# Optimization experiments

Measured on AMD Instinct MI355X. Metric: run time of the kernel, lower is better.

Reference implementation:

```python
import jax, jax.numpy as jnp
import numpy as np

B, T, D, H, NB, K, CDIM, CTX = 8, 4096, 3, 128, 6, 20, 128, 7


def setup_inputs() -> dict:
    key = jax.random.key(0)
    ks = jax.random.split(key, 16)
    s = 0.05
    inp = {
        'p': jax.random.normal(ks[0], (B, T, D), jnp.float32),
        'W_pos': jax.random.normal(ks[1], (D, H), jnp.float32) * s,
        'b_pos': jnp.zeros((H,), jnp.float32),
        # ResnetBlockFC(2H -> H): fc_0(2H,H), fc_1(H,H), shortcut(2H,H, no bias)
        'blk_W0': jax.random.normal(ks[2], (NB, 2 * H, H), jnp.float32) * s,
        'blk_b0': jnp.zeros((NB, H), jnp.float32),
        'blk_W1': jax.random.normal(ks[3], (NB, H, H), jnp.float32) * s,
        'blk_b1': jnp.zeros((NB, H), jnp.float32),
        'blk_Ws': jax.random.normal(ks[4], (NB, 2 * H, H), jnp.float32) * s,
        # Attention: score MLP on context (dim 7 -> 1), output proj (H -> H)
        'att_Wc': jax.random.normal(ks[5], (NB, CTX, 1), jnp.float32) * s,
        'att_bc': jnp.zeros((NB, 1), jnp.float32),
        'att_Wo': jax.random.normal(ks[6], (NB, H, H), jnp.float32) * s,
        'att_bo': jnp.zeros((NB, H), jnp.float32),
        'W_c': jax.random.normal(ks[7], (H, CDIM), jnp.float32) * s,
        'b_c': jnp.zeros((CDIM,), jnp.float32),
    }
    return inp


def _knn(p):
    # squared pairwise distances [B,T,T], top-K smallest
    sq = jnp.sum(p * p, axis=-1)  # [B,T]
    d2 = sq[:, :, None] + sq[:, None, :] - 2.0 * jnp.einsum('btd,bsd->bts', p, p)
    neg, idx = jax.lax.top_k(-d2, K)            # idx: [B,T,K]
    dis = jnp.sqrt(jnp.maximum(-neg, 1e-12))    # euclidean distance [B,T,K]
    return dis, idx


def _gather(c, idx):
    # c: [B,T,h], idx: [B,T,K] -> [B,T,K,h]  (vectorized pool_local)
    return jax.vmap(lambda ci, ii: ci[ii])(c, idx)


def _resnet_block(x, W0, b0, W1, b1, Ws):
    # occupancy-networks ResnetBlockFC: shortcut(x) + fc_1(relu(fc_0(relu(x))))
    h = jnp.maximum(x, 0.0) @ W0 + b0
    dx = jnp.maximum(h, 0.0) @ W1 + b1
    return x @ Ws + dx


def reference(p, W_pos, b_pos, blk_W0, blk_b0, blk_W1, blk_b1, blk_Ws,
              att_Wc, att_bc, att_Wo, att_bo, W_c, b_c):
    dis, idx = _knn(p)
    pooled_points = _gather(p, idx)                                   # [B,T,K,3]
    p_rep = jnp.broadcast_to(p[:, :, None, :], (B, T, K, D))
    context = jnp.concatenate([dis[..., None], pooled_points, p_rep], axis=-1)  # [B,T,K,7]

    net = p @ W_pos + b_pos                                           # [B,T,H]
    last_net = jnp.zeros_like(net)
    for i in range(NB):
        pooled = _gather(net, idx)                                    # [B,T,K,H]
        # attention over the K neighbors, weights from context
        scores = context @ att_Wc[i] + att_bc[i]                      # [B,T,K,1]
        w = jax.nn.softmax(scores, axis=2)
        att = jnp.sum(w * pooled, axis=2) @ att_Wo[i] + att_bo[i]     # [B,T,H]
        x = jnp.concatenate([net, att], axis=2)                       # [B,T,2H]
        net = _resnet_block(x, blk_W0[i], blk_b0[i], blk_W1[i], blk_b1[i], blk_Ws[i])
        net = net + last_net
        last_net = net
    return net @ W_c + b_c                                            # [B,T,c_dim]
```

## Files before the change

kernel.cpp:

```cpp
#include <hip/hip_runtime.h>
#include <hip/hip_bf16.h>
#include <math.h>

#define BB 8
#define TT 4096
#define HHD 128
#define NBK 6
#define KNN 20
#define BT (BB*TT)

typedef __attribute__((ext_vector_type(8))) short bf16x8;
typedef __attribute__((ext_vector_type(4))) float f32x4;

__device__ __forceinline__ float b2f(unsigned short u){
  return __uint_as_float(((unsigned int)u) << 16);
}
__device__ __forceinline__ unsigned short f2b(float f){
  unsigned int x = __float_as_uint(f);
  unsigned int r = (x + 0x7fffu + ((x >> 16) & 1u)) >> 16;
  return (unsigned short)r;
}
__device__ __forceinline__ float ldp(const void* base, int i, int f32m){
  return f32m ? ((const float*)base)[i] : b2f(((const unsigned short*)base)[i]);
}
__device__ __forceinline__ float lo2f(unsigned int u){ return __uint_as_float(u << 16); }
__device__ __forceinline__ float hi2f(unsigned int u){ return __uint_as_float(u & 0xffff0000u); }
__device__ __forceinline__ unsigned int relu2(unsigned int u){
  unsigned int s = u & 0x80008000u;
  unsigned int m = s | (s - (s >> 15));
  return u & ~m;
}
__device__ __forceinline__ bf16x8 relu8(bf16x8 x){
  union { bf16x8 v; unsigned int u[4]; } t; t.v = x;
  t.u[0] = relu2(t.u[0]); t.u[1] = relu2(t.u[1]);
  t.u[2] = relu2(t.u[2]); t.u[3] = relu2(t.u[3]);
  return t.v;
}

__global__ void k_detect(const unsigned short* __restrict__ wpos_raw, int* __restrict__ flag){
  int lane = threadIdx.x;
  int cnt = 0;
  for (int i = lane; i < 384; i += 64) {
    unsigned int e = (wpos_raw[i] >> 7) & 0xFFu;
    if (e >= 0x90u) cnt++;
  }
  #pragma unroll
  for (int off = 32; off > 0; off >>= 1) cnt += __shfl_down(cnt, off);
  if (lane == 0) *flag = (cnt > 10) ? 1 : 0;
}

__global__ __launch_bounds__(256) void k_prep_points(const void* __restrict__ p,
                                                     const int* __restrict__ flagp,
                                                     float4* __restrict__ pf4){
  int r = blockIdx.x*256 + threadIdx.x;
  if (r >= BT) return;
  int f32m = *flagp;
  float x = ldp(p, r*3+0, f32m), y = ldp(p, r*3+1, f32m), z = ldp(p, r*3+2, f32m);
  float sq = __fadd_rn(__fadd_rn(__fmul_rn(x,x), __fmul_rn(y,y)), __fmul_rn(z,z));
  pf4[r] = make_float4(x, y, z, sq);
}

__global__ __launch_bounds__(256) void k_net0(const float4* __restrict__ pf4,
                                              const void* __restrict__ Wpos,
                                              const void* __restrict__ bpos,
                                              const int* __restrict__ flagp,
                                              unsigned short* __restrict__ netA){
  int t = blockIdx.x*256 + threadIdx.x;
  int f32m = *flagp;
  int c = t & 127, r = t >> 7;
  float4 q = pf4[r];
  float v = ldp(bpos, c, f32m);
  v = fmaf(q.x, ldp(Wpos, c,       f32m), v);
  v = fmaf(q.y, ldp(Wpos, 128 + c, f32m), v);
  v = fmaf(q.z, ldp(Wpos, 256 + c, f32m), v);
  netA[t] = f2b(v);
}

__global__ __launch_bounds__(256) void k_transpose(const void* __restrict__ W0,
                                                   const void* __restrict__ W1,
                                                   const void* __restrict__ Ws,
                                                   const void* __restrict__ Wo,
                                                   const void* __restrict__ Wc,
                                                   const int* __restrict__ flagp,
                                                   unsigned short* __restrict__ wT){
  int t = blockIdx.x*256 + threadIdx.x;
  int f32m = *flagp;
  if (t < 196608) {
    int i = t >> 15; int rem = t & 32767; int n = rem >> 8; int k = rem & 255;
    wT[t] = f2b(ldp(W0, i*32768 + k*128 + n, f32m));
  } else if (t < 294912) {
    int u = t - 196608; int i = u >> 14; int rem = u & 16383; int n = rem >> 7; int k = rem & 127;
    wT[t] = f2b(ldp(W1, i*16384 + k*128 + n, f32m));
  } else if (t < 491520) {
    int u = t - 294912; int i = u >> 15; int rem = u & 32767; int n = rem >> 8; int k = rem & 255;
    wT[t] = f2b(ldp(Ws, i*32768 + k*128 + n, f32m));
  } else if (t < 589824) {
    int u = t - 491520; int i = u >> 14; int rem = u & 16383; int n = rem >> 7; int k = rem & 127;
    wT[t] = f2b(ldp(Wo, i*16384 + k*128 + n, f32m));
  } else if (t < 606208) {
    int u = t - 589824; int n = u >> 7; int k = u & 127;
    wT[t] = f2b(ldp(Wc, k*128 + n, f32m));
  }
}

#define INS(act, dv, iv) do { bool A_ = (act); float D_ = (dv); int I_ = (iv);        \
  _Pragma("unroll")                                                                    \
  for (int j = 19; j >= 1; --j) {                                                      \
    bool cj = A_ && (D_ < ld[j]); bool cm = A_ && (D_ < ld[j-1]);                      \
    ld[j] = cj ? (cm ? ld[j-1] : D_) : ld[j];                                          \
    li[j] = cj ? (cm ? li[j-1] : I_) : li[j];                                          \
  }                                                                                    \
  { bool c0 = A_ && (D_ < ld[0]); ld[0] = c0 ? D_ : ld[0]; li[0] = c0 ? I_ : li[0]; } \
} while(0)

#define KCAP 22

__global__ __launch_bounds__(256) void k_knn(const float4* __restrict__ pf4,
                                             const void* __restrict__ Wc,
                                             const void* __restrict__ bc,
                                             const int* __restrict__ flagp,
                                             unsigned short* __restrict__ idx16,
                                             unsigned short* __restrict__ wsoftb){
  __shared__ __align__(16) char smem[16384 + KCAP*2048];
  __shared__ unsigned int sthr[64];
  float4* tile = (float4*)smem;
  float*  lsd  = (float*)smem;
  int*    lsi  = (int*)(smem + 20480);
  float2* stk  = (float2*)(smem + 16384);

  int tid  = threadIdx.x;
  int part = tid >> 6, lane = tid & 63;
  int rq   = blockIdx.x*64 + lane;
  int b    = rq >> 12;
  int f32m = *flagp;
  float4 q = pf4[rq];

  if (tid < 64) sthr[tid] = 0x7F7FFFFFu;

  float ld[20]; int li[20];
  #pragma unroll
  for (int j = 0; j < 20; ++j) { ld[j] = 3.0e38f; li[j] = 0; }
  float thresh = 3.0e38f;
  int cnt = 0;

  for (int ch = 0; ch < 4; ++ch) {
    __syncthreads();
    {
      const float4* src = pf4 + (b << 12) + part*1024 + ch*256;
      tile[part*256 + lane      ] = src[lane      ];
      tile[part*256 + lane +  64] = src[lane +  64];
      tile[part*256 + lane + 128] = src[lane + 128];
      tile[part*256 + lane + 192] = src[lane + 192];
    }
    __syncthreads();
    thresh = fminf(thresh, __uint_as_float(sthr[lane]));
    int baseI = part*1024 + ch*256;
    #pragma unroll 4
    for (int j = 0; j < 256; ++j) {
      float4 pt = tile[part*256 + j];
      float dot = __fadd_rn(__fadd_rn(__fmul_rn(q.x,pt.x), __fmul_rn(q.y,pt.y)),
                            __fmul_rn(q.z,pt.z));
      float d2  = __fsub_rn(__fadd_rn(q.w, pt.w), __fmul_rn(2.0f, dot));
      if (d2 < thresh) {
        stk[cnt*256 + tid] = make_float2(d2, __int_as_float(baseI + j));
        cnt++;
      }
      if (__ballot(cnt >= KCAP)) {
        #pragma unroll 1
        for (int u = 0; u < KCAP; ++u) {
          float2 e = stk[u*256 + tid];
          INS(u < cnt, e.x, __float_as_int(e.y));
        }
        cnt = 0;
        atomicMin(&sthr[lane], __float_as_uint(fmaxf(ld[19], 0.0f)));
        thresh = fminf(ld[19], __uint_as_float(sthr[lane]));
      }
    }
  }
  {
    int mc = cnt;
    #pragma unroll
    for (int o = 32; o > 0; o >>= 1) mc = max(mc, __shfl_xor(mc, o));
    #pragma unroll 1
    for (int u = 0; u < mc; ++u) {
      float2 e = stk[u*256 + tid];
      INS(u < cnt, e.x, __float_as_int(e.y));
    }
  }

  __syncthreads();
  #pragma unroll
  for (int j = 0; j < 20; ++j) { lsd[tid*20 + j] = ld[j]; lsi[tid*20 + j] = li[j]; }
  __syncthreads();

  if (tid < 64) {
    int p0 = tid*20, p1 = (64+tid)*20, p2 = (128+tid)*20, p3 = (192+tid)*20;
    int i0=0, i1=0, i2=0, i3=0;
    float dis[20]; int outi[20];
    #pragma unroll 4
    for (int o = 0; o < 20; ++o) {
      float d0 = lsd[p0+i0], d1 = lsd[p1+i1], d2v = lsd[p2+i2], d3 = lsd[p3+i3];
      float bd = d0; int sel = 0;
      if (d1  < bd) { bd = d1;  sel = 1; }
      if (d2v < bd) { bd = d2v; sel = 2; }
      if (d3  < bd) { bd = d3;  sel = 3; }
      int bi = (sel==0) ? lsi[p0+i0] : (sel==1) ? lsi[p1+i1] : (sel==2) ? lsi[p2+i2] : lsi[p3+i3];
      i0 += (sel==0); i1 += (sel==1); i2 += (sel==2); i3 += (sel==3);
      dis[o] = sqrtf(fmaxf(bd, 1e-12f));
      outi[o] = bi;
    }
    float nx[20], ny[20], nz[20];
    #pragma unroll 4
    for (int k = 0; k < 20; ++k) {
      idx16[rq*20 + k] = (unsigned short)outi[k];
      float4 pp = pf4[(b << 12) + outi[k]];
      nx[k] = pp.x; ny[k] = pp.y; nz[k] = pp.z;
    }
    for (int i = 0; i < NBK; ++i) {
      float w0 = ldp(Wc,i*7+0,f32m), w1 = ldp(Wc,i*7+1,f32m), w2 = ldp(Wc,i*7+2,f32m);
      float w3 = ldp(Wc,i*7+3,f32m), w4 = ldp(Wc,i*7+4,f32m), w5 = ldp(Wc,i*7+5,f32m);
      float w6 = ldp(Wc,i*7+6,f32m);
      float bci = ldp(bc,i,f32m);
      float s[20]; float mx = -3.0e38f;
      #pragma unroll
      for (int k = 0; k < 20; ++k) {
        float v = bci;
        v = fmaf(dis[k], w0, v);
        v = fmaf(nx[k], w1, v); v = fmaf(ny[k], w2, v); v = fmaf(nz[k], w3, v);
        v = fmaf(q.x, w4, v);  v = fmaf(q.y, w5, v);  v = fmaf(q.z, w6, v);
        s[k] = v; mx = fmaxf(mx, v);
      }
      float sum = 0.f;
      #pragma unroll
      for (int k = 0; k < 20; ++k) { float e = __expf(s[k] - mx); s[k] = e; sum += e; }
      float inv = 1.0f / sum;
      #pragma unroll
      for (int k = 0; k < 20; ++k) wsoftb[(rq*6 + i)*20 + k] = f2b(s[k]*inv);
    }
  }
}

__global__ __launch_bounds__(256) void k_block(const unsigned short* __restrict__ netIn,
                                               unsigned short* __restrict__ netOut,
                                               const unsigned short* __restrict__ idx16,
                                               const unsigned short* __restrict__ wsoftb,
                                               const unsigned short* __restrict__ wT,
                                               const void* __restrict__ b0s,
                                               const void* __restrict__ b1s,
                                               const void* __restrict__ bos,
                                               const int* __restrict__ flagp,
                                               int iblk, int hasResid){
  __shared__ unsigned short ldsA[2][16*136];
  __shared__ unsigned short ldsH[2][16*136];
  int tid = threadIdx.x;
  int f32m = *flagp;
  int w = tid >> 6, lane = tid & 63;
  int t = w >> 1;
  int c = w & 1;
  int b  = blockIdx.x & 7;
  int r0 = (b << 12) + ((blockIdx.x >> 3) << 5) + (t << 4);
  const unsigned short* W0T = wT + iblk*32768;
  const unsigned short* W1T = wT + 196608 + iblk*16384;
  const unsigned short* WsT = wT + 294912 + iblk*32768;
  const unsigned short* WoT = wT + 491520 + iblk*16384;
  int m = lane & 15, qd = lane >> 4;

  {
    int r = lane >> 2, cg = lane & 3;
    int grow = r0 + r;
    int cbase = c*64 + cg*16;
    const unsigned int* ip = (const unsigned int*)(idx16 + grow*20);
    const unsigned int* wp = (const unsigned int*)(wsoftb + (grow*6 + iblk)*20);
    unsigned int iv[10], wv[10];
    #pragma unroll
    for (int j = 0; j < 10; ++j) iv[j] = ip[j];
    #pragma unroll
    for (int j = 0; j < 10; ++j) wv[j] = wp[j];
    float acc[16];
    #pragma unroll
    for (int j = 0; j < 16; ++j) acc[j] = 0.f;
    #pragma unroll 4
    for (int k = 0; k < 20; ++k) {
      unsigned int pair = iv[k >> 1];
      int nb = (int)((k & 1) ? (pair >> 16) : pair) & 4095;
      unsigned int wpair = wv[k >> 1];
      float wk = (k & 1) ? hi2f(wpair) : lo2f(wpair);
      const uint4* np_ = (const uint4*)(netIn + ((b << 12) + nb)*128 + cbase);
      #pragma unroll
      for (int u = 0; u < 2; ++u) {
        uint4 uu = np_[u];
        acc[u*8+0] = fmaf(wk, lo2f(uu.x), acc[u*8+0]);
        acc[u*8+1] = fmaf(wk, hi2f(uu.x), acc[u*8+1]);
        acc[u*8+2] = fmaf(wk, lo2f(uu.y), acc[u*8+2]);
        acc[u*8+3] = fmaf(wk, hi2f(uu.y), acc[u*8+3]);
        acc[u*8+4] = fmaf(wk, lo2f(uu.z), acc[u*8+4]);
        acc[u*8+5] = fmaf(wk, hi2f(uu.z), acc[u*8+5]);
        acc[u*8+6] = fmaf(wk, lo2f(uu.w), acc[u*8+6]);
        acc[u*8+7] = fmaf(wk, hi2f(uu.w), acc[u*8+7]);
      }
    }
    unsigned short* hb = ldsH[t];
    #pragma unroll
    for (int j = 0; j < 8; ++j) {
      unsigned int pr = ((unsigned int)f2b(acc[2*j+1]) << 16) | (unsigned int)f2b(acc[2*j]);
      *(unsigned int*)(hb + r*136 + cbase + 2*j) = pr;
    }
  }
  __syncthreads();

  {
    bf16x8 asf[4];
    #pragma unroll
    for (int ks = 0; ks < 4; ++ks)
      asf[ks] = *(const bf16x8*)(ldsH[t] + m*136 + ks*32 + qd*8);
    f32x4 acc2[4];
    #pragma unroll
    for (int i = 0; i < 4; ++i) { f32x4 z = {0.f,0.f,0.f,0.f}; acc2[i] = z; }
    #pragma unroll
    for (int i = 0; i < 4; ++i) {
      int cti = c*4 + i;
      const unsigned short* bp = WoT + (cti*16 + m)*128 + qd*8;
      #pragma unroll
      for (int ks = 0; ks < 4; ++ks)
        acc2[i] = __builtin_amdgcn_mfma_f32_16x16x32_bf16(asf[ks], *(const bf16x8*)(bp + ks*32), acc2[i], 0, 0, 0);
    }
    unsigned short* ab = ldsA[t];
    #pragma unroll
    for (int i = 0; i < 4; ++i) {
      int col = (c*4 + i)*16 + m;
      float bo = ldp(bos, iblk*128 + col, f32m);
      #pragma unroll
      for (int rr = 0; rr < 4; ++rr)
        ab[(qd*4 + rr)*136 + col] = f2b(acc2[i][rr] + bo);
    }
  }
  __syncthreads();

  bf16x8 nf[4], af[4];
  {
    const unsigned short* nrow = netIn + (r0 + m)*128;
    #pragma unroll
    for (int ks = 0; ks < 4; ++ks) nf[ks] = *(const bf16x8*)(nrow + ks*32 + qd*8);
    #pragma unroll
    for (int ks = 0; ks < 4; ++ks) af[ks] = *(const bf16x8*)(ldsA[t] + m*136 + ks*32 + qd*8);
    bf16x8 rnf[4], raf[4];
    #pragma unroll
    for (int ks = 0; ks < 4; ++ks) { rnf[ks] = relu8(nf[ks]); raf[ks] = relu8(af[ks]); }
    f32x4 acc3[4];
    #pragma unroll
    for (int i = 0; i < 4; ++i) { f32x4 z = {0.f,0.f,0.f,0.f}; acc3[i] = z; }
    #pragma unroll
    for (int i = 0; i < 4; ++i) {
      int cti = c*4 + i;
      const unsigned short* bp = W0T + (cti*16 + m)*256 + qd*8;
      #pragma unroll
      for (int ks = 0; ks < 4; ++ks)
        acc3[i] = __builtin_amdgcn_mfma_f32_16x16x32_bf16(rnf[ks], *(const bf16x8*)(bp + ks*32), acc3[i], 0, 0, 0);
      #pragma unroll
      for (int ks = 0; ks < 4; ++ks)
        acc3[i] = __builtin_amdgcn_mfma_f32_16x16x32_bf16(raf[ks], *(const bf16x8*)(bp + 128 + ks*32), acc3[i], 0, 0, 0);
    }
    unsigned short* hb = ldsH[t];
    #pragma unroll
    for (int i = 0; i < 4; ++i) {
      int col = (c*4 + i)*16 + m;
      float b0v = ldp(b0s, iblk*128 + col, f32m);
      #pragma unroll
      for (int rr = 0; rr < 4; ++rr)
        hb[(qd*4 + rr)*136 + col] = f2b(fmaxf(acc3[i][rr] + b0v, 0.f));
    }
  }
  __syncthreads();

  {
    bf16x8 hf[4];
    #pragma unroll
    for (int ks = 0; ks < 4; ++ks) hf[ks] = *(const bf16x8*)(ldsH[t] + m*136 + ks*32 + qd*8);
    f32x4 acc4[4];
    #pragma unroll
    for (int i = 0; i < 4; ++i) { f32x4 z = {0.f,0.f,0.f,0.f}; acc4[i] = z; }
    #pragma unroll
    for (int i = 0; i < 4; ++i) {
      int cti = c*4 + i;
      const unsigned short* bp1 = W1T + (cti*16 + m)*128 + qd*8;
      #pragma unroll
      for (int ks = 0; ks < 4; ++ks)
        acc4[i] = __builtin_amdgcn_mfma_f32_16x16x32_bf16(hf[ks], *(const bf16x8*)(bp1 + ks*32), acc4[i], 0, 0, 0);
      const unsigned short* bps = WsT + (cti*16 + m)*256 + qd*8;
      #pragma unroll
      for (int ks = 0; ks < 4; ++ks)
        acc4[i] = __builtin_amdgcn_mfma_f32_16x16x32_bf16(nf[ks], *(const bf16x8*)(bps + ks*32), acc4[i], 0, 0, 0);
      #pragma unroll
      for (int ks = 0; ks < 4; ++ks)
        acc4[i] = __builtin_amdgcn_mfma_f32_16x16x32_bf16(af[ks], *(const bf16x8*)(bps + 128 + ks*32), acc4[i], 0, 0, 0);
    }
    #pragma unroll
    for (int i = 0; i < 4; ++i) {
      int col = (c*4 + i)*16 + m;
      float b1v = ldp(b1s, iblk*128 + col, f32m);
      #pragma unroll
      for (int rr = 0; rr < 4; ++rr) {
        int grow2 = r0 + qd*4 + rr;
        float v = acc4[i][rr] + b1v;
        if (hasResid) v += b2f(netIn[grow2*128 + col]);
        netOut[grow2*128 + col] = f2b(v);
      }
    }
  }
}

__global__ __launch_bounds__(256) void k_final(const unsigned short* __restrict__ netIn,
                                               const unsigned short* __restrict__ WcT,
                                               const void* __restrict__ bcv,
                                               const int* __restrict__ flagp,
                                               void* __restrict__ out){
  int tid = threadIdx.x; int w = tid >> 6, lane = tid & 63;
  int f32m = *flagp;
  int t = w >> 1, c = w & 1;
  int r0 = blockIdx.x*32 + t*16;
  int m = lane & 15, qd = lane >> 4;
  bf16x8 nf[4];
  #pragma unroll
  for (int ks = 0; ks < 4; ++ks)
    nf[ks] = *(const bf16x8*)(netIn + (r0 + m)*128 + ks*32 + qd*8);
  f32x4 acc[4];
  #pragma unroll
  for (int i = 0; i < 4; ++i) { f32x4 z = {0.f,0.f,0.f,0.f}; acc[i] = z; }
  #pragma unroll
  for (int i = 0; i < 4; ++i) {
    int cti = c*4 + i;
    const unsigned short* bp = WcT + (cti*16 + m)*128 + qd*8;
    #pragma unroll
    for (int ks = 0; ks < 4; ++ks)
      acc[i] = __builtin_amdgcn_mfma_f32_16x16x32_bf16(nf[ks], *(const bf16x8*)(bp + ks*32), acc[i], 0, 0, 0);
  }
  if (f32m) {
    float* o = (float*)out;
    #pragma unroll
    for (int i = 0; i < 4; ++i) {
      int col = (c*4 + i)*16 + m;
      float bcf = ldp(bcv, col, 1);
      #pragma unroll
      for (int rr = 0; rr < 4; ++rr)
        o[(r0 + qd*4 + rr)*128 + col] = acc[i][rr] + bcf;
    }
  } else {
    unsigned short* o = (unsigned short*)out;
    #pragma unroll
    for (int i = 0; i < 4; ++i) {
      int col = (c*4 + i)*16 + m;
      float bcf = ldp(bcv, col, 0);
      #pragma unroll
      for (int rr = 0; rr < 4; ++rr)
        o[(r0 + qd*4 + rr)*128 + col] = f2b(acc[i][rr] + bcf);
    }
  }
}

extern "C" void kernel_launch(void* const* d_in, const int* in_sizes, int n_in,
                              void* d_out, int out_size, void* d_ws, size_t ws_size,
                              hipStream_t stream){
  const void* p    = d_in[0];
  const void* Wpos = d_in[1];
  const void* bpos = d_in[2];
  const void* W0   = d_in[3];
  const void* b0   = d_in[4];
  const void* W1   = d_in[5];
  const void* b1   = d_in[6];
  const void* Ws   = d_in[7];
  const void* Wc_  = d_in[8];
  const void* bc_  = d_in[9];
  const void* Wo   = d_in[10];
  const void* bo   = d_in[11];
  const void* WC   = d_in[12];
  const void* bC   = d_in[13];

  char* ws = (char*)d_ws;
  int*            flag   = (int*)(ws + 0);
  float4*         pf4    = (float4*)(ws + 256);
  unsigned short* idx16  = (unsigned short*)(ws + 524544);
  unsigned short* wsoftb = (unsigned short*)(ws + 1835264);
  unsigned short* netA   = (unsigned short*)(ws + 9699584);
  unsigned short* wT     = (unsigned short*)(ws + 18088192);

  k_detect     <<<dim3(1),     dim3(64),  0, stream>>>((const unsigned short*)Wpos, flag);
  k_prep_points<<<dim3(128),   dim3(256), 0, stream>>>(p, flag, pf4);
  k_net0       <<<dim3(16384), dim3(256), 0, stream>>>(pf4, Wpos, bpos, flag, netA);
  k_transpose  <<<dim3(2368),  dim3(256), 0, stream>>>(W0, W1, Ws, Wo, WC, flag, wT);
  k_knn        <<<dim3(512),   dim3(256), 0, stream>>>(pf4, Wc_, bc_, flag, idx16, wsoftb);

  unsigned short* a   = netA;
  unsigned short* bpt = (unsigned short*)d_out;
  for (int i = 0; i < 6; ++i) {
    k_block<<<dim3(1024), dim3(256), 0, stream>>>(a, bpt, idx16, wsoftb, wT,
                                                  b0, b1, bo, flag, i, (i > 0) ? 1 : 0);
    unsigned short* t = a; a = bpt; bpt = t;
  }
  k_final<<<dim3(1024), dim3(256), 0, stream>>>(a, wT + 589824, bC, flag, d_out);
}
```

Before: 646.0 us.

## Split KNN candidate scan across eight wave partitions with compact LDS stacks

The KNN kernel now runs 512 threads per block, so each query's 4096 candidates are scanned by eight waves of 512 points instead of four waves of 1024, halving the serial scan per thread. The candidate stack is split into separate float distance and 16-bit index arrays with a smaller capacity. The flush check now runs once per four candidates, so the stack fills half as often. The final merge becomes 8-way, and shared memory is repacked to fit in about 62 KB. The trade-offs are a longer merge, more LDS per block, and more frequent stack flushes from the smaller capacity.

```diff
diff --git a/kernel.cpp b/kernel.cpp
--- a/kernel.cpp
+++ b/kernel.cpp
@@ -113,20 +113,21 @@
   { bool c0 = A_ && (D_ < ld[0]); ld[0] = c0 ? D_ : ld[0]; li[0] = c0 ? I_ : li[0]; } \
 } while(0)
 
-#define KCAP 22
-
-__global__ __launch_bounds__(256) void k_knn(const float4* __restrict__ pf4,
+#define KCAP 10
+
+__global__ __launch_bounds__(512) void k_knn(const float4* __restrict__ pf4,
                                              const void* __restrict__ Wc,
                                              const void* __restrict__ bc,
                                              const int* __restrict__ flagp,
                                              unsigned short* __restrict__ idx16,
                                              unsigned short* __restrict__ wsoftb){
-  __shared__ __align__(16) char smem[16384 + KCAP*2048];
+  __shared__ __align__(16) char smem[63488];
   __shared__ unsigned int sthr[64];
-  float4* tile = (float4*)smem;
-  float*  lsd  = (float*)smem;
-  int*    lsi  = (int*)(smem + 20480);
-  float2* stk  = (float2*)(smem + 16384);
+  float4*         tile  = (float4*)smem;
+  float*          stkd  = (float*)(smem + 32768);
+  unsigned short* stki  = (unsigned short*)(smem + 53248);
+  float*          lsd   = (float*)smem;
+  unsigned short* lsi16 = (unsigned short*)(smem + 40960);
 
   int tid  = threadIdx.x;
   int part = tid >> 6, lane = tid & 63;
@@ -143,10 +144,10 @@
   float thresh = 3.0e38f;
   int cnt = 0;
 
-  for (int ch = 0; ch < 4; ++ch) {
+  for (int ch = 0; ch < 2; ++ch) {
     __syncthreads();
     {
-      const float4* src = pf4 + (b << 12) + part*1024 + ch*256;
+      const float4* src = pf4 + (b << 12) + part*512 + ch*256;
       tile[part*256 + lane      ] = src[lane      ];
       tile[part*256 + lane +  64] = src[lane +  64];
       tile[part*256 + lane + 128] = src[lane + 128];
@@ -154,22 +155,27 @@
     }
     __syncthreads();
     thresh = fminf(thresh, __uint_as_float(sthr[lane]));
-    int baseI = part*1024 + ch*256;
-    #pragma unroll 4
-    for (int j = 0; j < 256; ++j) {
-      float4 pt = tile[part*256 + j];
-      float dot = __fadd_rn(__fadd_rn(__fmul_rn(q.x,pt.x), __fmul_rn(q.y,pt.y)),
-                            __fmul_rn(q.z,pt.z));
-      float d2  = __fsub_rn(__fadd_rn(q.w, pt.w), __fmul_rn(2.0f, dot));
-      if (d2 < thresh) {
-        stk[cnt*256 + tid] = make_float2(d2, __int_as_float(baseI + j));
-        cnt++;
+    int baseI = part*512 + ch*256;
+    for (int j0 = 0; j0 < 256; j0 += 4) {
+      #pragma unroll
+      for (int jj = 0; jj < 4; ++jj) {
+        int j = j0 + jj;
+        float4 pt = tile[part*256 + j];
+        float dot = __fadd_rn(__fadd_rn(__fmul_rn(q.x,pt.x), __fmul_rn(q.y,pt.y)),
+                              __fmul_rn(q.z,pt.z));
+        float d2  = __fsub_rn(__fadd_rn(q.w, pt.w), __fmul_rn(2.0f, dot));
+        if (d2 < thresh) {
+          stkd[cnt*512 + tid] = d2;
+          stki[cnt*512 + tid] = (unsigned short)(baseI + j);
+          cnt++;
+        }
       }
-      if (__ballot(cnt >= KCAP)) {
+      if (__ballot(cnt >= KCAP-3)) {
         #pragma unroll 1
         for (int u = 0; u < KCAP; ++u) {
-          float2 e = stk[u*256 + tid];
-          INS(u < cnt, e.x, __float_as_int(e.y));
+          float dv = stkd[u*512 + tid];
+          int   iv = (int)stki[u*512 + tid];
+          INS(u < cnt, dv, iv);
         }
         cnt = 0;
         atomicMin(&sthr[lane], __float_as_uint(fmaxf(ld[19], 0.0f)));
@@ -183,29 +189,40 @@
     for (int o = 32; o > 0; o >>= 1) mc = max(mc, __shfl_xor(mc, o));
     #pragma unroll 1
     for (int u = 0; u < mc; ++u) {
-      float2 e = stk[u*256 + tid];
-      INS(u < cnt, e.x, __float_as_int(e.y));
+      float dv = stkd[u*512 + tid];
+      int   iv = (int)stki[u*512 + tid];
+      INS(u < cnt, dv, iv);
     }
   }
 
   __syncthreads();
   #pragma unroll
-  for (int j = 0; j < 20; ++j) { lsd[tid*20 + j] = ld[j]; lsi[tid*20 + j] = li[j]; }
+  for (int j = 0; j < 20; ++j) { lsd[tid*20 + j] = ld[j]; lsi16[tid*20 + j] = (unsigned short)li[j]; }
   __syncthreads();
 
   if (tid < 64) {
-    int p0 = tid*20, p1 = (64+tid)*20, p2 = (128+tid)*20, p3 = (192+tid)*20;
-    int i0=0, i1=0, i2=0, i3=0;
+    int p0 = tid*20,        p1 = ( 64+tid)*20, p2 = (128+tid)*20, p3 = (192+tid)*20;
+    int p4 = (256+tid)*20,  p5 = (320+tid)*20, p6 = (384+tid)*20, p7 = (448+tid)*20;
+    int i0=0,i1=0,i2=0,i3=0,i4=0,i5=0,i6=0,i7=0;
     float dis[20]; int outi[20];
     #pragma unroll 4
     for (int o = 0; o < 20; ++o) {
       float d0 = lsd[p0+i0], d1 = lsd[p1+i1], d2v = lsd[p2+i2], d3 = lsd[p3+i3];
+      float d4 = lsd[p4+i4], d5 = lsd[p5+i5], d6v = lsd[p6+i6], d7 = lsd[p7+i7];
       float bd = d0; int sel = 0;
       if (d1  < bd) { bd = d1;  sel = 1; }
       if (d2v < bd) { bd = d2v; sel = 2; }
       if (d3  < bd) { bd = d3;  sel = 3; }
-      int bi = (sel==0) ? lsi[p0+i0] : (sel==1) ? lsi[p1+i1] : (sel==2) ? lsi[p2+i2] : lsi[p3+i3];
+      if (d4  < bd) { bd = d4;  sel = 4; }
+      if (d5  < bd) { bd = d5;  sel = 5; }
+      if (d6v < bd) { bd = d6v; sel = 6; }
+      if (d7  < bd) { bd = d7;  sel = 7; }
+      int off = (sel < 4)
+        ? ((sel < 2) ? (sel == 0 ? p0+i0 : p1+i1) : (sel == 2 ? p2+i2 : p3+i3))
+        : ((sel < 6) ? (sel == 4 ? p4+i4 : p5+i5) : (sel == 6 ? p6+i6 : p7+i7));
+      int bi = (int)lsi16[off];
       i0 += (sel==0); i1 += (sel==1); i2 += (sel==2); i3 += (sel==3);
+      i4 += (sel==4); i5 += (sel==5); i6 += (sel==6); i7 += (sel==7);
       dis[o] = sqrtf(fmaxf(bd, 1e-12f));
       outi[o] = bi;
     }
@@ -487,7 +504,7 @@
   k_prep_points<<<dim3(128),   dim3(256), 0, stream>>>(p, flag, pf4);
   k_net0       <<<dim3(16384), dim3(256), 0, stream>>>(pf4, Wpos, bpos, flag, netA);
   k_transpose  <<<dim3(2368),  dim3(256), 0, stream>>>(W0, W1, Ws, Wo, WC, flag, wT);
-  k_knn        <<<dim3(512),   dim3(256), 0, stream>>>(pf4, Wc_, bc_, flag, idx16, wsoftb);
+  k_knn        <<<dim3(512),   dim3(512), 0, stream>>>(pf4, Wc_, bc_, flag, idx16, wsoftb);
 
   unsigned short* a   = netA;
   unsigned short* bpt = (unsigned short*)d_out;
```

After: 743.2 us. +15.0%, slower.

## Compute kNN candidate distances with bf16 split MFMA and exact fp32 rescoring

Applied to the files above, without the earlier changes.

The kNN distance scan moves from scalar fp32 per-thread loops to MFMA 16x16x32 bf16 instructions. Point coordinates and query terms are split into hi/lo bf16 pairs to approximate fp32 precision. Candidates under the threshold plus a safety margin are pushed to a stack, then recomputed exactly in fp32 during flush before top-K insertion. Work is remapped so each wave covers 16 queries across 4 k-groups, and the final merge gains an index tie-break. This cuts ALU work in the dominant O(T^2) scan, at the cost of more candidates passing the loosened threshold and more frequent flushes.

```diff
diff --git a/kernel.cpp b/kernel.cpp
--- a/kernel.cpp
+++ b/kernel.cpp
@@ -35,6 +35,12 @@
   t.u[0] = relu2(t.u[0]); t.u[1] = relu2(t.u[1]);
   t.u[2] = relu2(t.u[2]); t.u[3] = relu2(t.u[3]);
   return t.v;
+}
+__device__ __forceinline__ unsigned int splitpk(float v){
+  unsigned short h = f2b(v);
+  float hv = b2f(h);
+  unsigned short l = f2b(v - hv);
+  return (unsigned int)h | ((unsigned int)l << 16);
 }
 
 __global__ void k_detect(const unsigned short* __restrict__ wpos_raw, int* __restrict__ flag){
@@ -113,7 +119,28 @@
   { bool c0 = A_ && (D_ < ld[0]); ld[0] = c0 ? D_ : ld[0]; li[0] = c0 ? I_ : li[0]; } \
 } while(0)
 
-#define KCAP 22
+#define KCAP   20
+#define MARGIN 0.02f
+
+#define KNN_FLUSH() do {                                                               \
+  int mc_ = cnt;                                                                       \
+  _Pragma("unroll")                                                                    \
+  for (int o_ = 32; o_ > 0; o_ >>= 1) { int t_ = __shfl_xor(mc_, o_); mc_ = mc_ > t_ ? mc_ : t_; } \
+  _Pragma("unroll 1")                                                                  \
+  for (int u_ = 0; u_ < mc_; ++u_) {                                                   \
+    float2 e_ = stk[u_*256 + tid];                                                     \
+    bool act_ = u_ < cnt;                                                              \
+    int piv_ = __float_as_int(e_.y);                                                   \
+    float4 pp_ = tilef4[act_ ? (piv_ - ch*512) : 0];                                   \
+    float dot_ = __fadd_rn(__fadd_rn(__fmul_rn(q.x,pp_.x), __fmul_rn(q.y,pp_.y)),      \
+                           __fmul_rn(q.z,pp_.z));                                      \
+    float d2e_ = __fsub_rn(__fadd_rn(q.w, pp_.w), __fmul_rn(2.0f, dot_));              \
+    INS(act_, d2e_, piv_);                                                             \
+  }                                                                                    \
+  cnt = 0;                                                                             \
+  atomicMin(&sthr[qlocal], __float_as_uint(fmaxf(ld[19], 0.0f)));                      \
+  threshP = fminf(ld[19], __uint_as_float(sthr[qlocal])) + MARGIN;                     \
+} while(0)
 
 __global__ __launch_bounds__(256) void k_knn(const float4* __restrict__ pf4,
                                              const void* __restrict__ Wc,
@@ -121,71 +148,81 @@
                                              const int* __restrict__ flagp,
                                              unsigned short* __restrict__ idx16,
                                              unsigned short* __restrict__ wsoftb){
-  __shared__ __align__(16) char smem[16384 + KCAP*2048];
+  __shared__ __align__(16) char smem[57344];
   __shared__ unsigned int sthr[64];
-  float4* tile = (float4*)smem;
-  float*  lsd  = (float*)smem;
-  int*    lsi  = (int*)(smem + 20480);
-  float2* stk  = (float2*)(smem + 16384);
+  float4* tilef4 = (float4*)smem;
+  uint4*  tilesp = (uint4*)(smem + 8192);
+  float2* stk    = (float2*)(smem + 16384);
+  float*  lsd    = (float*)(smem + 16384);
+  int*    lsi    = (int*)(smem + 36864);
 
   int tid  = threadIdx.x;
-  int part = tid >> 6, lane = tid & 63;
-  int rq   = blockIdx.x*64 + lane;
-  int b    = rq >> 12;
+  int wv   = tid >> 6, lane = tid & 63;
+  int cq   = lane & 15;
+  int kg   = lane >> 4;
+  int qlocal = wv*16 + cq;
+  int b    = blockIdx.x >> 6;
   int f32m = *flagp;
-  float4 q = pf4[rq];
+  float4 q = pf4[blockIdx.x*64 + qlocal];
 
   if (tid < 64) sthr[tid] = 0x7F7FFFFFu;
+
+  union FRU { bf16x8 v; unsigned int u[4]; };
+  FRU bfr;
+  {
+    float e = (kg == 0) ? -2.0f*q.x : -2.0f*q.z;
+    unsigned int ehl = splitpk(e);
+    unsigned int eh = ehl & 0xffffu, el = ehl >> 16;
+    float f = (kg == 0) ? -2.0f*q.y : q.w;
+    unsigned int fhl = splitpk(f);
+    unsigned int fh = fhl & 0xffffu, fl = fhl >> 16;
+    unsigned int v0 = eh | (eh << 16);
+    unsigned int v1 = el | (el << 16);
+    unsigned int v2 = (kg == 0) ? (fh | (fh << 16)) : 0x3F803F80u;
+    unsigned int v3 = (kg == 0) ? (fl | (fl << 16)) : fhl;
+    if (kg >= 2) { v0 = 0; v1 = 0; v2 = 0; v3 = 0; }
+    bfr.u[0] = v0; bfr.u[1] = v1; bfr.u[2] = v2; bfr.u[3] = v3;
+  }
+  const f32x4 zf = {0.f, 0.f, 0.f, 0.f};
 
   float ld[20]; int li[20];
   #pragma unroll
   for (int j = 0; j < 20; ++j) { ld[j] = 3.0e38f; li[j] = 0; }
-  float thresh = 3.0e38f;
+  float threshP = 3.0e38f;
   int cnt = 0;
 
-  for (int ch = 0; ch < 4; ++ch) {
+  for (int ch = 0; ch < 8; ++ch) {
     __syncthreads();
     {
-      const float4* src = pf4 + (b << 12) + part*1024 + ch*256;
-      tile[part*256 + lane      ] = src[lane      ];
-      tile[part*256 + lane +  64] = src[lane +  64];
-      tile[part*256 + lane + 128] = src[lane + 128];
-      tile[part*256 + lane + 192] = src[lane + 192];
+      const float4* src = pf4 + (b << 12) + ch*512;
+      float4 a0 = src[tid], a1 = src[tid + 256];
+      tilef4[tid]       = a0;
+      tilef4[tid + 256] = a1;
+      tilesp[tid]       = make_uint4(splitpk(a0.x), splitpk(a0.y), splitpk(a0.z), splitpk(a0.w));
+      tilesp[tid + 256] = make_uint4(splitpk(a1.x), splitpk(a1.y), splitpk(a1.z), splitpk(a1.w));
     }
     __syncthreads();
-    thresh = fminf(thresh, __uint_as_float(sthr[lane]));
-    int baseI = part*1024 + ch*256;
+    threshP = fminf(ld[19], __uint_as_float(sthr[qlocal])) + MARGIN;
     #pragma unroll 4
-    for (int j = 0; j < 256; ++j) {
-      float4 pt = tile[part*256 + j];
-      float dot = __fadd_rn(__fadd_rn(__fmul_rn(q.x,pt.x), __fmul_rn(q.y,pt.y)),
-                            __fmul_rn(q.z,pt.z));
-      float d2  = __fsub_rn(__fadd_rn(q.w, pt.w), __fmul_rn(2.0f, dot));
-      if (d2 < thresh) {
-        stk[cnt*256 + tid] = make_float2(d2, __int_as_float(baseI + j));
-        cnt++;
+    for (int g = 0; g < 32; ++g) {
+      uint4 s = tilesp[g*16 + cq];
+      unsigned int u0 = (kg == 0) ? s.x : s.z;
+      unsigned int u2 = (kg == 0) ? s.y : s.w;
+      unsigned int u3 = (kg == 0) ? u2 : 0x3F803F80u;
+      if (kg >= 2) { u0 = 0; u2 = 0; u3 = 0; }
+      FRU afr; afr.u[0] = u0; afr.u[1] = u0; afr.u[2] = u2; afr.u[3] = u3;
+      f32x4 dd = __builtin_amdgcn_mfma_f32_16x16x32_bf16(afr.v, bfr.v, zf, 0, 0, 0);
+      int pbase = ch*512 + g*16 + kg*4;
+      #pragma unroll
+      for (int r = 0; r < 4; ++r) {
+        if (dd[r] < threshP) {
+          stk[cnt*256 + tid] = make_float2(dd[r], __int_as_float(pbase + r));
+          cnt++;
+        }
       }
-      if (__ballot(cnt >= KCAP)) {
-        #pragma unroll 1
-        for (int u = 0; u < KCAP; ++u) {
-          float2 e = stk[u*256 + tid];
-          INS(u < cnt, e.x, __float_as_int(e.y));
-        }
-        cnt = 0;
-        atomicMin(&sthr[lane], __float_as_uint(fmaxf(ld[19], 0.0f)));
-        thresh = fminf(ld[19], __uint_as_float(sthr[lane]));
-      }
-    }
-  }
-  {
-    int mc = cnt;
-    #pragma unroll
-    for (int o = 32; o > 0; o >>= 1) mc = max(mc, __shfl_xor(mc, o));
-    #pragma unroll 1
-    for (int u = 0; u < mc; ++u) {
-      float2 e = stk[u*256 + tid];
-      INS(u < cnt, e.x, __float_as_int(e.y));
-    }
+      if (__ballot(cnt >= KCAP-3)) KNN_FLUSH();
+    }
+    if (__ballot(cnt > 0)) KNN_FLUSH();
   }
 
   __syncthreads();
@@ -194,17 +231,21 @@
   __syncthreads();
 
   if (tid < 64) {
-    int p0 = tid*20, p1 = (64+tid)*20, p2 = (128+tid)*20, p3 = (192+tid)*20;
-    int i0=0, i1=0, i2=0, i3=0;
+    int w2 = tid >> 4, c2 = tid & 15;
+    int base = w2*64 + c2;
+    int p0 = base*20, p1 = (base+16)*20, p2 = (base+32)*20, p3 = (base+48)*20;
+    int i0 = 0, i1 = 0, i2 = 0, i3 = 0;
+    int rq = blockIdx.x*64 + tid;
+    float4 qq = pf4[rq];
     float dis[20]; int outi[20];
     #pragma unroll 4
     for (int o = 0; o < 20; ++o) {
       float d0 = lsd[p0+i0], d1 = lsd[p1+i1], d2v = lsd[p2+i2], d3 = lsd[p3+i3];
-      float bd = d0; int sel = 0;
-      if (d1  < bd) { bd = d1;  sel = 1; }
-      if (d2v < bd) { bd = d2v; sel = 2; }
-      if (d3  < bd) { bd = d3;  sel = 3; }
-      int bi = (sel==0) ? lsi[p0+i0] : (sel==1) ? lsi[p1+i1] : (sel==2) ? lsi[p2+i2] : lsi[p3+i3];
+      int   j0 = lsi[p0+i0], j1 = lsi[p1+i1], j2  = lsi[p2+i2], j3 = lsi[p3+i3];
+      float bd = d0; int bi = j0; int sel = 0;
+      if (d1  < bd || (d1  == bd && j1 < bi)) { bd = d1;  bi = j1; sel = 1; }
+      if (d2v < bd || (d2v == bd && j2 < bi)) { bd = d2v; bi = j2; sel = 2; }
+      if (d3  < bd || (d3  == bd && j3 < bi)) { bd = d3;  bi = j3; sel = 3; }
       i0 += (sel==0); i1 += (sel==1); i2 += (sel==2); i3 += (sel==3);
       dis[o] = sqrtf(fmaxf(bd, 1e-12f));
       outi[o] = bi;
@@ -227,7 +268,7 @@
         float v = bci;
         v = fmaf(dis[k], w0, v);
         v = fmaf(nx[k], w1, v); v = fmaf(ny[k], w2, v); v = fmaf(nz[k], w3, v);
-        v = fmaf(q.x, w4, v);  v = fmaf(q.y, w5, v);  v = fmaf(q.z, w6, v);
+        v = fmaf(qq.x, w4, v);  v = fmaf(qq.y, w5, v);  v = fmaf(qq.z, w6, v);
         s[k] = v; mx = fmaxf(mx, v);
       }
       float sum = 0.f;
```

New measurement: 613.2 us. 5.1% less time.
